# Kernel optimization log

Measured on AMD Instinct MI355X. Metric: run time of the kernel, lower is better.

Reference implementation:

```python
import jax, jax.numpy as jnp
import numpy as np

HEAD_SIZE = 128  # matches init head_size; original scales by global head_size**-0.5


def setup_inputs() -> dict:
    key = jax.random.key(0)
    k1, k2, k3, k4 = jax.random.split(key, 4)
    B, T, C, D = 16, 2048, 1024, HEAD_SIZE
    x = jax.random.normal(k1, (B, T, C), dtype=jnp.float32)
    # torch Linear weight is [out,in]; store transposed so forward is x @ W
    Wq = jax.random.normal(k2, (C, D), dtype=jnp.float32) * (C ** -0.5)
    Wk = jax.random.normal(k3, (C, D), dtype=jnp.float32) * (C ** -0.5)
    Wv = jax.random.normal(k4, (C, D), dtype=jnp.float32) * (C ** -0.5)
    return {"x": x, "Wq": Wq, "Wk": Wk, "Wv": Wv}


def reference(x, Wq, Wk, Wv):
    # x: [B,T,C]; projections -> [B,T,D]
    q = x @ Wq
    k = x @ Wk
    v = x @ Wv
    T = x.shape[1]
    scale = HEAD_SIZE ** -0.5
    # scores: [B,T,T]
    wei = jnp.einsum("btd,bsd->bts", q, k) * scale
    causal = jnp.tril(jnp.ones((T, T), dtype=bool))  # tril buffer
    wei = jnp.where(causal, wei, -jnp.inf)
    wei = jax.nn.softmax(wei, axis=-1)
    # dropout is identity in eval mode (deterministic reference)
    return wei @ v  # [B,T,D]
```

## Files before the change

kernel.cpp:

```cpp
#include <hip/hip_runtime.h>
#include <hip/hip_bf16.h>

typedef short bf16x8 __attribute__((ext_vector_type(8)));
typedef float f32x4 __attribute__((ext_vector_type(4)));
typedef unsigned short u16x4 __attribute__((ext_vector_type(4)));

#define B_ 16
#define T_ 2048
#define C_ 1024
#define D_ 128
#define M_ (B_ * T_)

static __device__ __forceinline__ unsigned short f2bf(float f) {
    unsigned int u = __builtin_bit_cast(unsigned int, f);
    unsigned int r = (u + 0x7fffu + ((u >> 16) & 1u)) >> 16;
    return (unsigned short)r;
}

__global__ void wt_kernel(const float* __restrict__ Wq, const float* __restrict__ Wk,
                          const float* __restrict__ Wv, unsigned short* __restrict__ Wt) {
    int idx = blockIdx.x * 256 + threadIdx.x;
    int o   = idx >> 17;
    int rem = idx & 131071;
    int k   = rem >> 7;
    int n   = rem & 127;
    const float* W = (o == 0) ? Wq : (o == 1) ? Wk : Wv;
    Wt[o * (D_ * C_) + n * C_ + k] = f2bf(W[rem]);
}

#define ASTR 68
#define BSTR 68

__launch_bounds__(512, 1)
__global__ void qkv_kernel(const float* __restrict__ x, const unsigned short* __restrict__ Wt,
                           unsigned short* __restrict__ Q, unsigned short* __restrict__ K,
                           unsigned short* __restrict__ Vt) {
    __shared__ unsigned short Alds[2][128 * ASTR];
    __shared__ unsigned short Blds[2][384 * BSTR];

    const int tid  = threadIdx.x;
    const int lane = tid & 63;
    const int w    = tid >> 6;
    const int wr   = w >> 2;
    const int wc   = w & 3;
    const int lr   = lane & 15;
    const int lk   = lane >> 4;
    const int m0   = blockIdx.x * 128;

    const int axr = tid >> 4;
    const int axc = (tid & 15) * 4;
    const int bxr = tid >> 3;
    const int bxc = (tid & 7) * 8;

    float4 ar[4];
    bf16x8 br[6];

    auto stage_load = [&](int k0) {
#pragma unroll
        for (int j = 0; j < 4; ++j)
            ar[j] = *(const float4*)(x + (size_t)(m0 + axr + j * 32) * C_ + k0 + axc);
#pragma unroll
        for (int j = 0; j < 6; ++j)
            br[j] = *(const bf16x8*)(Wt + (size_t)(bxr + j * 64) * C_ + k0 + bxc);
    };
    auto stage_write = [&](int buf) {
#pragma unroll
        for (int j = 0; j < 4; ++j) {
            u16x4 v;
            v[0] = f2bf(ar[j].x); v[1] = f2bf(ar[j].y);
            v[2] = f2bf(ar[j].z); v[3] = f2bf(ar[j].w);
            *(u16x4*)&Alds[buf][(axr + j * 32) * ASTR + axc] = v;
        }
#pragma unroll
        for (int j = 0; j < 6; ++j)
            *(bf16x8*)&Blds[buf][(bxr + j * 64) * BSTR + bxc] = br[j];
    };

    f32x4 acc[4][6] = {};

    auto compute = [&](int buf) {
#pragma unroll
        for (int kk = 0; kk < 2; ++kk) {
            bf16x8 a[4], b[6];
#pragma unroll
            for (int rb = 0; rb < 4; ++rb)
                a[rb] = *(bf16x8*)&Alds[buf][(wr * 64 + rb * 16 + lr) * ASTR + kk * 32 + lk * 8];
#pragma unroll
            for (int nb = 0; nb < 6; ++nb)
                b[nb] = *(bf16x8*)&Blds[buf][(wc * 96 + nb * 16 + lr) * BSTR + kk * 32 + lk * 8];
#pragma unroll
            for (int rb = 0; rb < 4; ++rb)
#pragma unroll
                for (int nb = 0; nb < 6; ++nb)
                    acc[rb][nb] = __builtin_amdgcn_mfma_f32_16x16x32_bf16(a[rb], b[nb], acc[rb][nb], 0, 0, 0);
        }
    };

    stage_load(0);
    stage_write(0);
    for (int t = 0; t < 16; ++t) {
        __syncthreads();
        if (t < 15) stage_load((t + 1) * 64);
        compute(t & 1);
        if (t < 15) stage_write((t + 1) & 1);
    }

    const float qscale = 0.08838834764831845f;
    const int b  = m0 / T_;
    const int t0 = m0 % T_;
#pragma unroll
    for (int rb = 0; rb < 4; ++rb) {
#pragma unroll
        for (int nb = 0; nb < 6; ++nb) {
            const int row0 = wr * 64 + rb * 16 + lk * 4;
            const int col  = wc * 96 + nb * 16 + lr;
            const int o    = col >> 7;
            const int d    = col & 127;
            f32x4 a = acc[rb][nb];
            if (o == 0) {
#pragma unroll
                for (int r = 0; r < 4; ++r)
                    Q[(size_t)(m0 + row0 + r) * D_ + d] = f2bf(a[r] * qscale);
            } else if (o == 1) {
#pragma unroll
                for (int r = 0; r < 4; ++r)
                    K[(size_t)(m0 + row0 + r) * D_ + d] = f2bf(a[r]);
            } else {
                u16x4 pv;
#pragma unroll
                for (int r = 0; r < 4; ++r) pv[r] = f2bf(a[r]);
                *(u16x4*)&Vt[((size_t)b * D_ + d) * T_ + t0 + row0] = pv;
            }
        }
    }
}

#define KSTR 132
#define VSTR 68
#define PSTR 68

__launch_bounds__(256, 2)
__global__ void attn_kernel(const unsigned short* __restrict__ Q, const unsigned short* __restrict__ K,
                            const unsigned short* __restrict__ Vt, float* __restrict__ out) {
    __shared__ unsigned short Klds[2][64 * KSTR];
    __shared__ unsigned short Vlds[2][128 * VSTR];
    __shared__ unsigned short Plds[4][16 * PSTR];

    const int tid  = threadIdx.x;
    const int lane = tid & 63;
    const int w    = tid >> 6;
    const int lr   = lane & 15;
    const int lk   = lane >> 4;

    const int batch = blockIdx.x >> 4;
    const int pair  = blockIdx.x & 15;

    const unsigned short* Qb = Q  + (size_t)batch * T_ * D_;
    const unsigned short* Kb = K  + (size_t)batch * T_ * D_;
    const unsigned short* Vb = Vt + (size_t)batch * D_ * T_;
    float* outb = out + (size_t)batch * T_ * D_;

    const int kxr = tid >> 4;
    const int kxc = (tid & 15) * 8;
    const int vxr = tid >> 3;
    const int vxc = (tid & 7) * 8;

    bf16x8 kr[4], vr[4];
    auto kv_load = [&](int kvt) {
        const int kv0 = kvt * 64;
#pragma unroll
        for (int j = 0; j < 4; ++j)
            kr[j] = *(const bf16x8*)(Kb + (size_t)(kv0 + kxr + j * 16) * D_ + kxc);
#pragma unroll
        for (int j = 0; j < 4; ++j)
            vr[j] = *(const bf16x8*)(Vb + (size_t)(vxr + j * 32) * T_ + kv0 + vxc);
    };
    auto kv_write = [&](int buf) {
#pragma unroll
        for (int j = 0; j < 4; ++j)
            *(bf16x8*)&Klds[buf][(kxr + j * 16) * KSTR + kxc] = kr[j];
#pragma unroll
        for (int j = 0; j < 4; ++j)
            *(bf16x8*)&Vlds[buf][(vxr + j * 32) * VSTR + vxc] = vr[j];
    };

    for (int half = 0; half < 2; ++half) {
        const int qt = (half == 0) ? pair : (31 - pair);
        const int qw = qt * 64 + w * 16;

        bf16x8 qf[4];
#pragma unroll
        for (int c = 0; c < 4; ++c)
            qf[c] = *(const bf16x8*)(Qb + (size_t)(qw + lr) * D_ + lk * 8 + c * 32);

        f32x4 o_acc[8] = {};
        float mrun[4] = {-1e30f, -1e30f, -1e30f, -1e30f};
        float lrun[4] = {0.f, 0.f, 0.f, 0.f};

        __syncthreads();
        kv_load(0);
        kv_write(0);

        for (int kvt = 0; kvt <= qt; ++kvt) {
            const int cur = kvt & 1;
            __syncthreads();
            if (kvt < qt) kv_load(kvt + 1);

            f32x4 s[4];
#pragma unroll
            for (int nb = 0; nb < 4; ++nb) {
                f32x4 a = {};
#pragma unroll
                for (int c = 0; c < 4; ++c) {
                    bf16x8 kf = *(bf16x8*)&Klds[cur][(nb * 16 + lr) * KSTR + lk * 8 + c * 32];
                    a = __builtin_amdgcn_mfma_f32_16x16x32_bf16(qf[c], kf, a, 0, 0, 0);
                }
                s[nb] = a;
            }

            if (kvt == qt) {
#pragma unroll
                for (int nb = 0; nb < 4; ++nb)
#pragma unroll
                    for (int r = 0; r < 4; ++r) {
                        int qg = qw + lk * 4 + r;
                        int kg = kvt * 64 + nb * 16 + lr;
                        if (kg > qg) s[nb][r] = -1e30f;
                    }
            }

            float scale_[4];
#pragma unroll
            for (int r = 0; r < 4; ++r) {
                float mx = fmaxf(fmaxf(s[0][r], s[1][r]), fmaxf(s[2][r], s[3][r]));
                mx = fmaxf(mx, __shfl_xor(mx, 1));
                mx = fmaxf(mx, __shfl_xor(mx, 2));
                mx = fmaxf(mx, __shfl_xor(mx, 4));
                mx = fmaxf(mx, __shfl_xor(mx, 8));
                float mnew = fmaxf(mrun[r], mx);
                scale_[r]  = __expf(mrun[r] - mnew);
                mrun[r]    = mnew;
                lrun[r]   *= scale_[r];
            }
#pragma unroll
            for (int db = 0; db < 8; ++db)
#pragma unroll
                for (int r = 0; r < 4; ++r) o_acc[db][r] *= scale_[r];

#pragma unroll
            for (int nb = 0; nb < 4; ++nb)
#pragma unroll
                for (int r = 0; r < 4; ++r) {
                    float p = __expf(s[nb][r] - mrun[r]);
                    lrun[r] += p;
                    Plds[w][(lk * 4 + r) * PSTR + nb * 16 + lr] = f2bf(p);
                }
            asm volatile("s_waitcnt lgkmcnt(0)" ::: "memory");
            __builtin_amdgcn_sched_barrier(0);

            bf16x8 pa[2];
#pragma unroll
            for (int c = 0; c < 2; ++c)
                pa[c] = *(bf16x8*)&Plds[w][lr * PSTR + lk * 8 + c * 32];
#pragma unroll
            for (int db = 0; db < 8; ++db) {
                f32x4 oo = o_acc[db];
#pragma unroll
                for (int c = 0; c < 2; ++c) {
                    bf16x8 vf = *(bf16x8*)&Vlds[cur][(db * 16 + lr) * VSTR + lk * 8 + c * 32];
                    oo = __builtin_amdgcn_mfma_f32_16x16x32_bf16(pa[c], vf, oo, 0, 0, 0);
                }
                o_acc[db] = oo;
            }

            if (kvt < qt) kv_write(cur ^ 1);
        }

#pragma unroll
        for (int r = 0; r < 4; ++r) {
            float sgm = lrun[r];
            sgm += __shfl_xor(sgm, 1);
            sgm += __shfl_xor(sgm, 2);
            sgm += __shfl_xor(sgm, 4);
            sgm += __shfl_xor(sgm, 8);
            lrun[r] = 1.0f / sgm;
        }
#pragma unroll
        for (int db = 0; db < 8; ++db)
#pragma unroll
            for (int r = 0; r < 4; ++r)
                outb[(size_t)(qw + lk * 4 + r) * D_ + db * 16 + lr] = o_acc[db][r] * lrun[r];
    }
}

extern "C" void kernel_launch(void* const* d_in, const int* in_sizes, int n_in,
                              void* d_out, int out_size, void* d_ws, size_t ws_size,
                              hipStream_t stream) {
    const float* x  = (const float*)d_in[0];
    const float* Wq = (const float*)d_in[1];
    const float* Wk = (const float*)d_in[2];
    const float* Wv = (const float*)d_in[3];

    unsigned short* Wt  = (unsigned short*)d_ws;
    unsigned short* Qw  = (unsigned short*)((char*)d_ws + (1 << 20));
    unsigned short* Kw  = Qw + (size_t)M_ * D_;
    unsigned short* Vtw = Kw + (size_t)M_ * D_;

    hipLaunchKernelGGL(wt_kernel, dim3(1536), dim3(256), 0, stream, Wq, Wk, Wv, Wt);
    hipLaunchKernelGGL(qkv_kernel, dim3(256), dim3(512), 0, stream, x, Wt, Qw, Kw, Vtw);
    hipLaunchKernelGGL(attn_kernel, dim3(256), dim3(256), 0, stream, Qw, Kw, Vtw, (float*)d_out);
}
```

Measured before the change: 101.4 us.

## Tile weight transpose, async-load B to LDS, split attention blocks per tile

The weight transpose kernel now stages a tile in LDS so both its reads and its bf16 writes are coalesced, and it writes a k-swizzled layout. The QKV GEMM loads the weight tile straight from global memory into unpadded, XOR-swizzled LDS using global_load_lds, which removes the register round trip and shrinks LDS so two blocks can fit per CU. The attention kernel no longer pairs a short and a long query tile in one block; it launches 512 blocks with one tile each, ordered short tiles first. This adds parallelism but gives up the built-in load balancing of the pairing.

```diff
diff --git a/kernel.cpp b/kernel.cpp
--- a/kernel.cpp
+++ b/kernel.cpp
@@ -17,26 +17,53 @@
     return (unsigned short)r;
 }
 
+static __device__ __forceinline__ void gll16(const unsigned short* g, unsigned short* l) {
+    __builtin_amdgcn_global_load_lds(
+        (const __attribute__((address_space(1))) void*)g,
+        (__attribute__((address_space(3))) void*)l, 16, 0, 0);
+}
+
+#define TPAD 133
+
 __global__ void wt_kernel(const float* __restrict__ Wq, const float* __restrict__ Wk,
                           const float* __restrict__ Wv, unsigned short* __restrict__ Wt) {
-    int idx = blockIdx.x * 256 + threadIdx.x;
-    int o   = idx >> 17;
-    int rem = idx & 131071;
-    int k   = rem >> 7;
-    int n   = rem & 127;
+    __shared__ float Tl[64 * TPAD];
+    const int o  = blockIdx.x >> 4;
+    const int k0 = (blockIdx.x & 15) * 64;
     const float* W = (o == 0) ? Wq : (o == 1) ? Wk : Wv;
-    Wt[o * (D_ * C_) + n * C_ + k] = f2bf(W[rem]);
+    const int tid = threadIdx.x;
+
+    const int kr = tid >> 5;
+    const int n4 = (tid & 31) * 4;
+#pragma unroll
+    for (int j = 0; j < 8; ++j) {
+        float4 v = *(const float4*)(W + (size_t)(k0 + kr + j * 8) * 128 + n4);
+        *(float4*)&Tl[(kr + j * 8) * TPAD + n4] = v;
+    }
+    __syncthreads();
+
+    const int nb = tid >> 3;
+    const int kg = (tid & 7) * 8;
+#pragma unroll
+    for (int j = 0; j < 4; ++j) {
+        const int nn = nb + j * 32;
+        const int kk = kg ^ ((nn & 7) * 8);
+        bf16x8 v;
+#pragma unroll
+        for (int e = 0; e < 8; ++e)
+            v[e] = (short)f2bf(Tl[(kk + e) * TPAD + nn]);
+        *(bf16x8*)&Wt[((size_t)o * 128 + nn) * 1024 + k0 + kg] = v;
+    }
 }
 
 #define ASTR 68
-#define BSTR 68
-
-__launch_bounds__(512, 1)
+
+__launch_bounds__(512, 2)
 __global__ void qkv_kernel(const float* __restrict__ x, const unsigned short* __restrict__ Wt,
                            unsigned short* __restrict__ Q, unsigned short* __restrict__ K,
                            unsigned short* __restrict__ Vt) {
     __shared__ unsigned short Alds[2][128 * ASTR];
-    __shared__ unsigned short Blds[2][384 * BSTR];
+    __shared__ unsigned short Blds[2][384 * 64];
 
     const int tid  = threadIdx.x;
     const int lane = tid & 63;
@@ -49,21 +76,14 @@
 
     const int axr = tid >> 4;
     const int axc = (tid & 15) * 4;
-    const int bxr = tid >> 3;
-    const int bxc = (tid & 7) * 8;
 
     float4 ar[4];
-    bf16x8 br[6];
-
-    auto stage_load = [&](int k0) {
+    auto loadA = [&](int k0) {
 #pragma unroll
         for (int j = 0; j < 4; ++j)
             ar[j] = *(const float4*)(x + (size_t)(m0 + axr + j * 32) * C_ + k0 + axc);
-#pragma unroll
-        for (int j = 0; j < 6; ++j)
-            br[j] = *(const bf16x8*)(Wt + (size_t)(bxr + j * 64) * C_ + k0 + bxc);
-    };
-    auto stage_write = [&](int buf) {
+    };
+    auto writeA = [&](int buf) {
 #pragma unroll
         for (int j = 0; j < 4; ++j) {
             u16x4 v;
@@ -71,9 +91,16 @@
             v[2] = f2bf(ar[j].z); v[3] = f2bf(ar[j].w);
             *(u16x4*)&Alds[buf][(axr + j * 32) * ASTR + axc] = v;
         }
-#pragma unroll
-        for (int j = 0; j < 6; ++j)
-            *(bf16x8*)&Blds[buf][(bxr + j * 64) * BSTR + bxc] = br[j];
+    };
+
+    auto stageB = [&](int k0, int buf) {
+#pragma unroll
+        for (int c = 0; c < 6; ++c) {
+            const int chunk = w * 6 + c;
+            const unsigned short* g = Wt + (size_t)(chunk * 8 + (lane >> 3)) * 1024
+                                         + k0 + (lane & 7) * 8;
+            gll16(g, &Blds[buf][chunk * 512]);
+        }
     };
 
     f32x4 acc[4][6] = {};
@@ -86,8 +113,10 @@
             for (int rb = 0; rb < 4; ++rb)
                 a[rb] = *(bf16x8*)&Alds[buf][(wr * 64 + rb * 16 + lr) * ASTR + kk * 32 + lk * 8];
 #pragma unroll
-            for (int nb = 0; nb < 6; ++nb)
-                b[nb] = *(bf16x8*)&Blds[buf][(wc * 96 + nb * 16 + lr) * BSTR + kk * 32 + lk * 8];
+            for (int nb = 0; nb < 6; ++nb) {
+                const int ng = wc * 96 + nb * 16 + lr;
+                b[nb] = *(bf16x8*)&Blds[buf][ng * 64 + ((kk * 32 + lk * 8) ^ ((ng & 7) * 8))];
+            }
 #pragma unroll
             for (int rb = 0; rb < 4; ++rb)
 #pragma unroll
@@ -96,13 +125,19 @@
         }
     };
 
-    stage_load(0);
-    stage_write(0);
+    stageB(0, 0);
+    loadA(0);
+    writeA(0);
+
     for (int t = 0; t < 16; ++t) {
         __syncthreads();
-        if (t < 15) stage_load((t + 1) * 64);
-        compute(t & 1);
-        if (t < 15) stage_write((t + 1) & 1);
+        const int cur = t & 1;
+        if (t < 15) {
+            stageB((t + 1) * 64, cur ^ 1);
+            loadA((t + 1) * 64);
+        }
+        compute(cur);
+        if (t < 15) writeA(cur ^ 1);
     }
 
     const float qscale = 0.08838834764831845f;
@@ -152,8 +187,10 @@
     const int lr   = lane & 15;
     const int lk   = lane >> 4;
 
-    const int batch = blockIdx.x >> 4;
-    const int pair  = blockIdx.x & 15;
+    int bid = blockIdx.x;
+    int batch, qt;
+    if (bid < 256) { batch = bid >> 4; qt = bid & 15; }
+    else           { bid -= 256; batch = bid >> 4; qt = 31 - (bid & 15); }
 
     const unsigned short* Qb = Q  + (size_t)batch * T_ * D_;
     const unsigned short* Kb = K  + (size_t)batch * T_ * D_;
@@ -184,113 +221,109 @@
             *(bf16x8*)&Vlds[buf][(vxr + j * 32) * VSTR + vxc] = vr[j];
     };
 
-    for (int half = 0; half < 2; ++half) {
-        const int qt = (half == 0) ? pair : (31 - pair);
-        const int qw = qt * 64 + w * 16;
-
-        bf16x8 qf[4];
-#pragma unroll
-        for (int c = 0; c < 4; ++c)
-            qf[c] = *(const bf16x8*)(Qb + (size_t)(qw + lr) * D_ + lk * 8 + c * 32);
-
-        f32x4 o_acc[8] = {};
-        float mrun[4] = {-1e30f, -1e30f, -1e30f, -1e30f};
-        float lrun[4] = {0.f, 0.f, 0.f, 0.f};
-
+    const int qw = qt * 64 + w * 16;
+
+    bf16x8 qf[4];
+#pragma unroll
+    for (int c = 0; c < 4; ++c)
+        qf[c] = *(const bf16x8*)(Qb + (size_t)(qw + lr) * D_ + lk * 8 + c * 32);
+
+    f32x4 o_acc[8] = {};
+    float mrun[4] = {-1e30f, -1e30f, -1e30f, -1e30f};
+    float lrun[4] = {0.f, 0.f, 0.f, 0.f};
+
+    kv_load(0);
+    kv_write(0);
+
+    for (int kvt = 0; kvt <= qt; ++kvt) {
+        const int cur = kvt & 1;
         __syncthreads();
-        kv_load(0);
-        kv_write(0);
-
-        for (int kvt = 0; kvt <= qt; ++kvt) {
-            const int cur = kvt & 1;
-            __syncthreads();
-            if (kvt < qt) kv_load(kvt + 1);
-
-            f32x4 s[4];
-#pragma unroll
-            for (int nb = 0; nb < 4; ++nb) {
-                f32x4 a = {};
-#pragma unroll
-                for (int c = 0; c < 4; ++c) {
-                    bf16x8 kf = *(bf16x8*)&Klds[cur][(nb * 16 + lr) * KSTR + lk * 8 + c * 32];
-                    a = __builtin_amdgcn_mfma_f32_16x16x32_bf16(qf[c], kf, a, 0, 0, 0);
+        if (kvt < qt) kv_load(kvt + 1);
+
+        f32x4 s[4];
+#pragma unroll
+        for (int nb = 0; nb < 4; ++nb) {
+            f32x4 a = {};
+#pragma unroll
+            for (int c = 0; c < 4; ++c) {
+                bf16x8 kf = *(bf16x8*)&Klds[cur][(nb * 16 + lr) * KSTR + lk * 8 + c * 32];
+                a = __builtin_amdgcn_mfma_f32_16x16x32_bf16(qf[c], kf, a, 0, 0, 0);
+            }
+            s[nb] = a;
+        }
+
+        if (kvt == qt) {
+#pragma unroll
+            for (int nb = 0; nb < 4; ++nb)
+#pragma unroll
+                for (int r = 0; r < 4; ++r) {
+                    int qg = qw + lk * 4 + r;
+                    int kg = kvt * 64 + nb * 16 + lr;
+                    if (kg > qg) s[nb][r] = -1e30f;
                 }
-                s[nb] = a;
-            }
-
-            if (kvt == qt) {
-#pragma unroll
-                for (int nb = 0; nb < 4; ++nb)
-#pragma unroll
-                    for (int r = 0; r < 4; ++r) {
-                        int qg = qw + lk * 4 + r;
-                        int kg = kvt * 64 + nb * 16 + lr;
-                        if (kg > qg) s[nb][r] = -1e30f;
-                    }
-            }
-
-            float scale_[4];
+        }
+
+        float scale_[4];
+#pragma unroll
+        for (int r = 0; r < 4; ++r) {
+            float mx = fmaxf(fmaxf(s[0][r], s[1][r]), fmaxf(s[2][r], s[3][r]));
+            mx = fmaxf(mx, __shfl_xor(mx, 1));
+            mx = fmaxf(mx, __shfl_xor(mx, 2));
+            mx = fmaxf(mx, __shfl_xor(mx, 4));
+            mx = fmaxf(mx, __shfl_xor(mx, 8));
+            float mnew = fmaxf(mrun[r], mx);
+            scale_[r]  = __expf(mrun[r] - mnew);
+            mrun[r]    = mnew;
+            lrun[r]   *= scale_[r];
+        }
+#pragma unroll
+        for (int db = 0; db < 8; ++db)
+#pragma unroll
+            for (int r = 0; r < 4; ++r) o_acc[db][r] *= scale_[r];
+
+#pragma unroll
+        for (int nb = 0; nb < 4; ++nb)
 #pragma unroll
             for (int r = 0; r < 4; ++r) {
-                float mx = fmaxf(fmaxf(s[0][r], s[1][r]), fmaxf(s[2][r], s[3][r]));
-                mx = fmaxf(mx, __shfl_xor(mx, 1));
-                mx = fmaxf(mx, __shfl_xor(mx, 2));
-                mx = fmaxf(mx, __shfl_xor(mx, 4));
-                mx = fmaxf(mx, __shfl_xor(mx, 8));
-                float mnew = fmaxf(mrun[r], mx);
-                scale_[r]  = __expf(mrun[r] - mnew);
-                mrun[r]    = mnew;
-                lrun[r]   *= scale_[r];
-            }
-#pragma unroll
-            for (int db = 0; db < 8; ++db)
-#pragma unroll
-                for (int r = 0; r < 4; ++r) o_acc[db][r] *= scale_[r];
-
-#pragma unroll
-            for (int nb = 0; nb < 4; ++nb)
-#pragma unroll
-                for (int r = 0; r < 4; ++r) {
-                    float p = __expf(s[nb][r] - mrun[r]);
-                    lrun[r] += p;
-                    Plds[w][(lk * 4 + r) * PSTR + nb * 16 + lr] = f2bf(p);
-                }
-            asm volatile("s_waitcnt lgkmcnt(0)" ::: "memory");
-            __builtin_amdgcn_sched_barrier(0);
-
-            bf16x8 pa[2];
-#pragma unroll
-            for (int c = 0; c < 2; ++c)
-                pa[c] = *(bf16x8*)&Plds[w][lr * PSTR + lk * 8 + c * 32];
-#pragma unroll
-            for (int db = 0; db < 8; ++db) {
-                f32x4 oo = o_acc[db];
-#pragma unroll
-                for (int c = 0; c < 2; ++c) {
-                    bf16x8 vf = *(bf16x8*)&Vlds[cur][(db * 16 + lr) * VSTR + lk * 8 + c * 32];
-                    oo = __builtin_amdgcn_mfma_f32_16x16x32_bf16(pa[c], vf, oo, 0, 0, 0);
-                }
-                o_acc[db] = oo;
-            }
-
-            if (kvt < qt) kv_write(cur ^ 1);
-        }
-
-#pragma unroll
-        for (int r = 0; r < 4; ++r) {
-            float sgm = lrun[r];
-            sgm += __shfl_xor(sgm, 1);
-            sgm += __shfl_xor(sgm, 2);
-            sgm += __shfl_xor(sgm, 4);
-            sgm += __shfl_xor(sgm, 8);
-            lrun[r] = 1.0f / sgm;
-        }
-#pragma unroll
-        for (int db = 0; db < 8; ++db)
-#pragma unroll
-            for (int r = 0; r < 4; ++r)
-                outb[(size_t)(qw + lk * 4 + r) * D_ + db * 16 + lr] = o_acc[db][r] * lrun[r];
-    }
+                float p = __expf(s[nb][r] - mrun[r]);
+                lrun[r] += p;
+                Plds[w][(lk * 4 + r) * PSTR + nb * 16 + lr] = f2bf(p);
+            }
+        asm volatile("s_waitcnt lgkmcnt(0)" ::: "memory");
+        __builtin_amdgcn_sched_barrier(0);
+
+        bf16x8 pa[2];
+#pragma unroll
+        for (int c = 0; c < 2; ++c)
+            pa[c] = *(bf16x8*)&Plds[w][lr * PSTR + lk * 8 + c * 32];
+#pragma unroll
+        for (int db = 0; db < 8; ++db) {
+            f32x4 oo = o_acc[db];
+#pragma unroll
+            for (int c = 0; c < 2; ++c) {
+                bf16x8 vf = *(bf16x8*)&Vlds[cur][(db * 16 + lr) * VSTR + lk * 8 + c * 32];
+                oo = __builtin_amdgcn_mfma_f32_16x16x32_bf16(pa[c], vf, oo, 0, 0, 0);
+            }
+            o_acc[db] = oo;
+        }
+
+        if (kvt < qt) kv_write(cur ^ 1);
+    }
+
+#pragma unroll
+    for (int r = 0; r < 4; ++r) {
+        float sgm = lrun[r];
+        sgm += __shfl_xor(sgm, 1);
+        sgm += __shfl_xor(sgm, 2);
+        sgm += __shfl_xor(sgm, 4);
+        sgm += __shfl_xor(sgm, 8);
+        lrun[r] = 1.0f / sgm;
+    }
+#pragma unroll
+    for (int db = 0; db < 8; ++db)
+#pragma unroll
+        for (int r = 0; r < 4; ++r)
+            outb[(size_t)(qw + lk * 4 + r) * D_ + db * 16 + lr] = o_acc[db][r] * lrun[r];
 }
 
 extern "C" void kernel_launch(void* const* d_in, const int* in_sizes, int n_in,
@@ -306,7 +339,7 @@
     unsigned short* Kw  = Qw + (size_t)M_ * D_;
     unsigned short* Vtw = Kw + (size_t)M_ * D_;
 
-    hipLaunchKernelGGL(wt_kernel, dim3(1536), dim3(256), 0, stream, Wq, Wk, Wv, Wt);
+    hipLaunchKernelGGL(wt_kernel, dim3(48), dim3(256), 0, stream, Wq, Wk, Wv, Wt);
     hipLaunchKernelGGL(qkv_kernel, dim3(256), dim3(512), 0, stream, x, Wt, Qw, Kw, Vtw);
-    hipLaunchKernelGGL(attn_kernel, dim3(256), dim3(256), 0, stream, Qw, Kw, Vtw, (float*)d_out);
-}
+    hipLaunchKernelGGL(attn_kernel, dim3(512), dim3(256), 0, stream, Qw, Kw, Vtw, (float*)d_out);
+}
```

Result: slower. 105.8 us (+4.3%).
